# Performance work log

Hardware: AMD Instinct MI355X
Metric: run time of the kernel (lower is better)

## Reference

```python
import jax, jax.numpy as jnp
import numpy as np

GRID = 8        # kornia equalize_clahe default grid_size=(8,8)
NUM_BINS = 256  # kornia default
CLIP_LIMIT = 40.0


def normalize_in_range(x, lo, hi):
    mn, mx = x.min(), x.max()
    return (x - mn) / (mx - mn) * (hi - lo) + lo


def equalize_clahe(x, clip_limit=CLIP_LIMIT, grid=GRID, bins=NUM_BINS):
    # x: (B, C, H, W) in [0, 1]; H, W divisible by grid
    B, C, H, W = x.shape
    th, tw = H // grid, W // grid
    pixels = th * tw

    # --- per-pixel bin index (histc with bins=256, min=0, max=1) ---
    bidx = jnp.clip((x * bins).astype(jnp.int32), 0, bins - 1)  # (B,C,H,W)

    # --- per-tile histograms via one segment_sum (scatter-add) ---
    ti = (jnp.arange(H) // th)[None, None, :, None]
    tj = (jnp.arange(W) // tw)[None, None, None, :]
    bb = jnp.arange(B)[:, None, None, None]
    cc = jnp.arange(C)[None, :, None, None]
    tile_id = ((bb * C + cc) * grid + ti) * grid + tj          # (B,C,H,W)
    flat = (tile_id * bins + bidx).reshape(-1)
    hist = jax.ops.segment_sum(
        jnp.ones(flat.shape, jnp.float32), flat,
        num_segments=B * C * grid * grid * bins,
    ).reshape(B, C, grid, grid, bins)

    # --- clip histogram and redistribute excess uniformly ---
    max_val = max(int(clip_limit * pixels // bins), 1)
    hist = jnp.minimum(hist, max_val)
    residual = (pixels - hist.sum(-1, keepdims=True)) / bins
    hist = hist + residual

    # --- CDF -> LUT (values in [0, bins-1], floored) ---
    lut = jnp.floor(jnp.clip(jnp.cumsum(hist, axis=-1) * ((bins - 1) / pixels),
                             0.0, bins - 1.0))                 # (B,C,gh,gw,bins)

    # --- bilinear interpolation between the 4 nearest tile LUTs ---
    gi = jnp.clip((jnp.arange(H) + 0.5) / th - 0.5, 0.0, grid - 1.0)
    gj = jnp.clip((jnp.arange(W) + 0.5) / tw - 0.5, 0.0, grid - 1.0)
    i0 = jnp.floor(gi).astype(jnp.int32); i1 = jnp.minimum(i0 + 1, grid - 1)
    j0 = jnp.floor(gj).astype(jnp.int32); j1 = jnp.minimum(j0 + 1, grid - 1)
    wy = (gi - i0)[None, None, :, None]
    wx = (gj - j0)[None, None, None, :]

    I0 = i0[None, None, :, None]; I1 = i1[None, None, :, None]
    J0 = j0[None, None, None, :]; J1 = j1[None, None, None, :]

    v00 = lut[bb, cc, I0, J0, bidx]
    v01 = lut[bb, cc, I0, J1, bidx]
    v10 = lut[bb, cc, I1, J0, bidx]
    v11 = lut[bb, cc, I1, J1, bidx]

    out = (1.0 - wy) * ((1.0 - wx) * v00 + wx * v01) + wy * ((1.0 - wx) * v10 + wx * v11)
    return out / (bins - 1)


def setup_inputs() -> dict:
    key = jax.random.key(0)
    kx, ky = jax.random.split(key)
    x = jax.random.normal(kx, (16, 1, 1024, 1024), dtype=jnp.float32)
    y = jax.random.randint(ky, (16,), 0, 10, dtype=jnp.int64)
    return {"x": x, "y": y}


def reference(x, y):
    x = normalize_in_range(x, 0.0, 1.0)
    mean = x.mean(axis=(0, 2, 3))
    std = jnp.std(x, axis=(0, 2, 3), ddof=1)  # torch unbiased std
    x = (x - mean[None, :, None, None]) / std[None, :, None, None]
    x = normalize_in_range(x, 0.0, 1.0)
    x = equalize_clahe(x, clip_limit=40.0)
    return (x, y)
```

## Files before the change

kernel.cpp:

```cpp
#include <hip/hip_runtime.h>


#define BINS 256
#define FBINS 2048
#define MAXV 2560u

__global__ __launch_bounds__(256, 4) void k_tilestat(const float* __restrict__ x,
                                                     float2* __restrict__ partials,
                                                     unsigned* __restrict__ finehg){
  __shared__ unsigned fh[FBINS];
  __shared__ float smin[4], smax[4];
  __shared__ float sp[2];
  int t = threadIdx.x;
  int tile = blockIdx.x;
  int bc = tile >> 6, ti = (tile >> 3) & 7, tj = tile & 7;
  const float4* x4 = (const float4*)(x + ((size_t)bc * 1024 + ti * 128) * 1024 + tj * 128);
  float4 v[16];
  #pragma unroll
  for (int k = 0; k < 16; k++){
    int p = t + (k << 8);
    v[k] = x4[(p >> 5) * 256 + (p & 31)];
  }
  #pragma unroll
  for (int i = 0; i < FBINS / 256; i++) fh[t + i * 256] = 0u;
  float lmin = INFINITY, lmax = -INFINITY;
  #pragma unroll
  for (int k = 0; k < 16; k++){
    lmin = fminf(lmin, fminf(fminf(v[k].x, v[k].y), fminf(v[k].z, v[k].w)));
    lmax = fmaxf(lmax, fmaxf(fmaxf(v[k].x, v[k].y), fmaxf(v[k].z, v[k].w)));
  }
  for (int o = 32; o > 0; o >>= 1){
    lmin = fminf(lmin, __shfl_down(lmin, o, 64));
    lmax = fmaxf(lmax, __shfl_down(lmax, o, 64));
  }
  int lane = t & 63, wv = t >> 6;
  if (lane == 0){ smin[wv] = lmin; smax[wv] = lmax; }
  __syncthreads();
  if (t == 0){
    float m = smin[0], M = smax[0];
    #pragma unroll
    for (int i = 1; i < 4; i++){ m = fminf(m, smin[i]); M = fmaxf(M, smax[i]); }
    partials[tile] = make_float2(m, M);
    sp[0] = m;
    sp[1] = (float)FBINS / fmaxf(M - m, 1e-30f);
  }
  __syncthreads();
  float tmn = sp[0], tinv = sp[1];
  #pragma unroll
  for (int k = 0; k < 16; k++){
    int b0 = min((int)((v[k].x - tmn) * tinv), FBINS - 1);
    int b1 = min((int)((v[k].y - tmn) * tinv), FBINS - 1);
    int b2 = min((int)((v[k].z - tmn) * tinv), FBINS - 1);
    int b3 = min((int)((v[k].w - tmn) * tinv), FBINS - 1);
    atomicAdd(&fh[b0], 1u);
    atomicAdd(&fh[b1], 1u);
    atomicAdd(&fh[b2], 1u);
    atomicAdd(&fh[b3], 1u);
  }
  __syncthreads();
  unsigned* outp = finehg + (size_t)tile * (FBINS / 2);
  #pragma unroll
  for (int i = 0; i < FBINS / 512; i++){
    int w = t + i * 256;
    outp[w] = (fh[2 * w] & 0xFFFFu) | (fh[2 * w + 1] << 16);
  }
}

__global__ __launch_bounds__(256) void k_lut(const float2* __restrict__ partials,
                                             int nparts,
                                             const unsigned* __restrict__ finehg,
                                             float* __restrict__ lut,
                                             float2* __restrict__ gmm,
                                             const int* __restrict__ y,
                                             float* __restrict__ out,
                                             int N, int tail){
  __shared__ unsigned ch[BINS];
  __shared__ unsigned wsum[4];
  __shared__ float smin[4], smax[4];
  __shared__ float sp[2];
  int t = threadIdx.x;
  int tile = blockIdx.x;
  int lane = t & 63, wv = t >> 6;
  ch[t] = 0u;
  float lmin = INFINITY, lmax = -INFINITY;
  for (int i = t; i < nparts; i += 256){
    float2 p = partials[i];
    lmin = fminf(lmin, p.x);
    lmax = fmaxf(lmax, p.y);
  }
  for (int o = 32; o > 0; o >>= 1){
    lmin = fminf(lmin, __shfl_down(lmin, o, 64));
    lmax = fmaxf(lmax, __shfl_down(lmax, o, 64));
  }
  if (lane == 0){ smin[wv] = lmin; smax[wv] = lmax; }
  __syncthreads();
  if (t == 0){
    float m = smin[0], M = smax[0];
    #pragma unroll
    for (int i = 1; i < 4; i++){ m = fminf(m, smin[i]); M = fmaxf(M, smax[i]); }
    sp[0] = m;
    sp[1] = 1.0f / (M - m);
  }
  __syncthreads();
  float mn = sp[0], inv = sp[1];
  float2 tp = partials[tile];
  float tw = (tp.y - tp.x) * (1.0f / (float)FBINS);
  const uint4* fhp4 = (const uint4*)(finehg + (size_t)tile * (FBINS / 2));
  uint4 pk = fhp4[t];
  unsigned c[8];
  c[0] = pk.x & 0xFFFFu; c[1] = pk.x >> 16;
  c[2] = pk.y & 0xFFFFu; c[3] = pk.y >> 16;
  c[4] = pk.z & 0xFFFFu; c[5] = pk.z >> 16;
  c[6] = pk.w & 0xFFFFu; c[7] = pk.w >> 16;
  int f0 = t << 3;
  unsigned acc = 0;
  int cur = -1;
  #pragma unroll
  for (int i = 0; i < 8; i++){
    if (!c[i]) continue;
    float ctr = tp.x + ((float)(f0 + i) + 0.5f) * tw;
    int cb = min(max((int)(((ctr - mn) * inv) * 256.0f), 0), 255);
    if (cb != cur){
      if (acc) atomicAdd(&ch[cur], acc);
      acc = 0u;
      cur = cb;
    }
    acc += c[i];
  }
  if (acc) atomicAdd(&ch[cur], acc);
  __syncthreads();
  unsigned h = ch[t];
  if (h > MAXV) h = MAXV;
  unsigned s = h;
  #pragma unroll
  for (int o = 1; o < 64; o <<= 1){
    unsigned nb = __shfl_up(s, o, 64);
    if (lane >= o) s += nb;
  }
  if (lane == 63) wsum[wv] = s;
  __syncthreads();
  unsigned off = 0;
  #pragma unroll
  for (int i = 0; i < 3; i++) if (i < wv) off += wsum[i];
  unsigned total = wsum[0] + wsum[1] + wsum[2] + wsum[3];
  float residual = (16384.0f - (float)total) * (1.0f / 256.0f);
  float cum = ((float)(s + off) + (float)(t + 1) * residual) * (255.0f / 16384.0f);
  lut[(size_t)tile * BINS + t] = floorf(fminf(fmaxf(cum, 0.0f), 255.0f));
  if (tile == 0){
    if (t == 0) *gmm = make_float2(mn, inv);
    if (t < tail) out[N + t] = (float)y[t];
  }
}

__global__ __launch_bounds__(256) void k_apply(const float* __restrict__ x,
                                               const float2* __restrict__ gmm,
                                               const float* __restrict__ lutg,
                                               float* __restrict__ out){
  __shared__ float2 lint[2048];
  int t = threadIdx.x;
  int strip = blockIdx.x;
  int b = strip >> 7;
  int r0 = (strip & 127) << 3;
  float gi = fminf(fmaxf((r0 + 0.5f) * (1.0f / 128.0f) - 0.5f, 0.0f), 7.0f);
  int i0 = (int)gi;
  int i1 = min(i0 + 1, 7);
  const float* g0 = lutg + ((size_t)b * 8 + i0) * 2048;
  const float* g1 = lutg + ((size_t)b * 8 + i1) * 2048;
  #pragma unroll
  for (int i = 0; i < 8; i++){
    int k = t + i * 256;
    lint[k] = make_float2(g0[k], g1[k]);
  }
  float2 mmv = *gmm;
  float mn = mmv.x, inv = mmv.y;
  int j0[4], j1[4];
  float wx[4];
  #pragma unroll
  for (int c = 0; c < 4; c++){
    int col = (t << 2) + c;
    float gj = fminf(fmaxf((col + 0.5f) * (1.0f / 128.0f) - 0.5f, 0.0f), 7.0f);
    j0[c] = (int)gj;
    j1[c] = min(j0[c] + 1, 7);
    wx[c] = gj - (float)j0[c];
  }
  size_t base4 = ((size_t)b * 1024 + r0) * 256;
  __syncthreads();
  #pragma unroll
  for (int r = 0; r < 8; r++){
    int h = r0 + r;
    float giw = fminf(fmaxf((h + 0.5f) * (1.0f / 128.0f) - 0.5f, 0.0f), 7.0f);
    float wy = giw - (float)i0;
    float4 xv = ((const float4*)x)[base4 + r * 256 + t];
    int bi[4];
    bi[0] = min(max((int)(((xv.x - mn) * inv) * 256.0f), 0), 255);
    bi[1] = min(max((int)(((xv.y - mn) * inv) * 256.0f), 0), 255);
    bi[2] = min(max((int)(((xv.z - mn) * inv) * 256.0f), 0), 255);
    bi[3] = min(max((int)(((xv.w - mn) * inv) * 256.0f), 0), 255);
    float res[4];
    #pragma unroll
    for (int c = 0; c < 4; c++){
      float2 p0 = lint[(j0[c] << 8) + bi[c]];
      float2 p1 = lint[(j1[c] << 8) + bi[c]];
      float top = p0.x + wx[c] * (p1.x - p0.x);
      float bot = p0.y + wx[c] * (p1.y - p0.y);
      res[c] = (top + wy * (bot - top)) * (1.0f / 255.0f);
    }
    ((float4*)out)[base4 + r * 256 + t] = make_float4(res[0], res[1], res[2], res[3]);
  }
}

extern "C" void kernel_launch(void* const* d_in, const int* in_sizes, int n_in,
                              void* d_out, int out_size, void* d_ws, size_t ws_size,
                              hipStream_t stream){
  const float* x = (const float*)d_in[0];
  const int* y = (const int*)d_in[1];
  float* out = (float*)d_out;
  int N = in_sizes[0];
  int B = N >> 20;
  int T = B * 64;
  float2* partials = (float2*)d_ws;
  float2* gmm = (float2*)((char*)d_ws + 8192);
  unsigned* fineh = (unsigned*)((char*)d_ws + 16384);
  float* lut = (float*)((char*)d_ws + 16384 + (size_t)T * (FBINS * 2));
  int tail = out_size - N;

  hipLaunchKernelGGL(k_tilestat, dim3(T), dim3(256), 0, stream, x, partials, fineh);
  hipLaunchKernelGGL(k_lut, dim3(T), dim3(256), 0, stream,
                     partials, T, fineh, lut, gmm, y, out, N, tail);
  hipLaunchKernelGGL(k_apply, dim3(B * 128), dim3(256), 0, stream,
                     x, gmm, lut, out);
}
```

Baseline: 130.3 us.

## Store LUTs as bytes and pack four neighbor-tile entries per word in LDS

The LUT is now written as uint8 instead of float. The apply kernel packs the four neighbouring tile LUT values (i0/i1 × j0/j1) for each bin into one 32-bit LDS word, so each pixel needs one LDS read instead of two float2 reads. This cuts LUT global traffic and LDS bandwidth, at the cost of byte-granular global loads during staging and extra shift/convert ALU work per pixel.

Result: no change. 130.3 us (-0.0%).

```diff
diff --git a/kernel.cpp b/kernel.cpp
--- a/kernel.cpp
+++ b/kernel.cpp
@@ -69,7 +69,7 @@
 __global__ __launch_bounds__(256) void k_lut(const float2* __restrict__ partials,
                                              int nparts,
                                              const unsigned* __restrict__ finehg,
-                                             float* __restrict__ lut,
+                                             unsigned char* __restrict__ lut,
                                              float2* __restrict__ gmm,
                                              const int* __restrict__ y,
                                              float* __restrict__ out,
@@ -145,7 +145,8 @@
   unsigned total = wsum[0] + wsum[1] + wsum[2] + wsum[3];
   float residual = (16384.0f - (float)total) * (1.0f / 256.0f);
   float cum = ((float)(s + off) + (float)(t + 1) * residual) * (255.0f / 16384.0f);
-  lut[(size_t)tile * BINS + t] = floorf(fminf(fmaxf(cum, 0.0f), 255.0f));
+  lut[(size_t)tile * BINS + t] =
+      (unsigned char)(int)floorf(fminf(fmaxf(cum, 0.0f), 255.0f));
   if (tile == 0){
     if (t == 0) *gmm = make_float2(mn, inv);
     if (t < tail) out[N + t] = (float)y[t];
@@ -154,9 +155,9 @@
 
 __global__ __launch_bounds__(256) void k_apply(const float* __restrict__ x,
                                                const float2* __restrict__ gmm,
-                                               const float* __restrict__ lutg,
+                                               const unsigned char* __restrict__ lutg,
                                                float* __restrict__ out){
-  __shared__ float2 lint[2048];
+  __shared__ unsigned pkl[2048];
   int t = threadIdx.x;
   int strip = blockIdx.x;
   int b = strip >> 7;
@@ -164,23 +165,26 @@
   float gi = fminf(fmaxf((r0 + 0.5f) * (1.0f / 128.0f) - 0.5f, 0.0f), 7.0f);
   int i0 = (int)gi;
   int i1 = min(i0 + 1, 7);
-  const float* g0 = lutg + ((size_t)b * 8 + i0) * 2048;
-  const float* g1 = lutg + ((size_t)b * 8 + i1) * 2048;
-  #pragma unroll
-  for (int i = 0; i < 8; i++){
-    int k = t + i * 256;
-    lint[k] = make_float2(g0[k], g1[k]);
+  const unsigned char* g0 = lutg + ((size_t)b * 8 + i0) * 2048;
+  const unsigned char* g1 = lutg + ((size_t)b * 8 + i1) * 2048;
+  #pragma unroll
+  for (int e = 0; e < 8; e++){
+    int e1 = min(e + 1, 7);
+    unsigned r00 = g0[e * 256 + t];
+    unsigned r10 = g1[e * 256 + t];
+    unsigned r01 = g0[e1 * 256 + t];
+    unsigned r11 = g1[e1 * 256 + t];
+    pkl[e * 256 + t] = r00 | (r10 << 8) | (r01 << 16) | (r11 << 24);
   }
   float2 mmv = *gmm;
   float mn = mmv.x, inv = mmv.y;
-  int j0[4], j1[4];
+  int j0[4];
   float wx[4];
   #pragma unroll
   for (int c = 0; c < 4; c++){
     int col = (t << 2) + c;
     float gj = fminf(fmaxf((col + 0.5f) * (1.0f / 128.0f) - 0.5f, 0.0f), 7.0f);
     j0[c] = (int)gj;
-    j1[c] = min(j0[c] + 1, 7);
     wx[c] = gj - (float)j0[c];
   }
   size_t base4 = ((size_t)b * 1024 + r0) * 256;
@@ -199,10 +203,13 @@
     float res[4];
     #pragma unroll
     for (int c = 0; c < 4; c++){
-      float2 p0 = lint[(j0[c] << 8) + bi[c]];
-      float2 p1 = lint[(j1[c] << 8) + bi[c]];
-      float top = p0.x + wx[c] * (p1.x - p0.x);
-      float bot = p0.y + wx[c] * (p1.y - p0.y);
+      unsigned pk = pkl[(j0[c] << 8) + bi[c]];
+      float f00 = (float)(pk & 255u);
+      float f10 = (float)((pk >> 8) & 255u);
+      float f01 = (float)((pk >> 16) & 255u);
+      float f11 = (float)(pk >> 24);
+      float top = f00 + wx[c] * (f01 - f00);
+      float bot = f10 + wx[c] * (f11 - f10);
       res[c] = (top + wy * (bot - top)) * (1.0f / 255.0f);
     }
     ((float4*)out)[base4 + r * 256 + t] = make_float4(res[0], res[1], res[2], res[3]);
@@ -221,7 +228,7 @@
   float2* partials = (float2*)d_ws;
   float2* gmm = (float2*)((char*)d_ws + 8192);
   unsigned* fineh = (unsigned*)((char*)d_ws + 16384);
-  float* lut = (float*)((char*)d_ws + 16384 + (size_t)T * (FBINS * 2));
+  unsigned char* lut = (unsigned char*)((char*)d_ws + 16384 + (size_t)T * (FBINS * 2));
   int tail = out_size - N;
 
   hipLaunchKernelGGL(k_tilestat, dim3(T), dim3(256), 0, stream, x, partials, fineh);
```
